# Optimization experiments

Hardware: AMD Instinct MI355X
Metric: run time of the kernel (lower is better)

## Reference

```python
import jax, jax.numpy as jnp
import numpy as np

D_MODEL = 1024
NUM_Q_HEADS = 16
NUM_KV_HEADS = 4
HEAD_DIM = D_MODEL // NUM_Q_HEADS  # 64
B, T = 4, 2048


def _rotate(x):
    # interleaved rotate-half: (x1, x2) pairs -> (-x2, x1)
    x1 = x[..., ::2]
    x2 = x[..., 1::2]
    return jnp.stack((-x2, x1), axis=-1).reshape(x.shape)


def setup_inputs() -> dict:
    key = jax.random.key(0)
    ks = jax.random.split(key, 6)
    x = jax.random.normal(ks[0], (B, T, D_MODEL), dtype=jnp.float32)
    # RoPE tables (precomputed buffers): [T, head_dim]
    pos = jnp.arange(T, dtype=jnp.float32)[:, None]
    inv_freq = 1.0 / (10000.0 ** (jnp.arange(0, HEAD_DIM, 2, dtype=jnp.float32) / HEAD_DIM))
    ang = pos * inv_freq[None, :]                      # [T, head_dim//2]
    ang = jnp.repeat(ang, 2, axis=-1)                  # [T, head_dim]
    cos, sin = jnp.cos(ang), jnp.sin(ang)
    # Linear weights stored as [in, out] (torch y = x @ W.T with W:[out,in]);
    # xavier-uniform scale for a square d_model x d_model layer
    lim = float(np.sqrt(6.0 / (2 * D_MODEL)))
    Wq = jax.random.uniform(ks[1], (D_MODEL, D_MODEL), jnp.float32, -lim, lim)
    kv_out = 2 * NUM_KV_HEADS * HEAD_DIM
    lim_kv = float(np.sqrt(6.0 / (D_MODEL + kv_out)))
    Wkv = jax.random.uniform(ks[2], (D_MODEL, kv_out), jnp.float32, -lim_kv, lim_kv)
    Wo = jax.random.uniform(ks[3], (D_MODEL, D_MODEL), jnp.float32, -lim, lim)
    return {"x": x, "cos": cos, "sin": sin, "Wq": Wq, "Wkv": Wkv, "Wo": Wo}


def reference(x, cos, sin, Wq, Wkv, Wo):
    Bx, Tx, C = x.shape
    hd = HEAD_DIM
    scale = hd ** -0.5
    # projections
    q = (x @ Wq).reshape(Bx, Tx, NUM_Q_HEADS, hd).transpose(0, 2, 1, 3)   # [B,Hq,T,hd]
    kv = (x @ Wkv).reshape(Bx, Tx, NUM_KV_HEADS, 2, hd)
    k = kv[..., 0, :].transpose(0, 2, 1, 3)                               # [B,Hkv,T,hd]
    v = kv[..., 1, :].transpose(0, 2, 1, 3)
    rf = NUM_Q_HEADS // NUM_KV_HEADS
    k = jnp.repeat(k, rf, axis=1)                                         # [B,Hq,T,hd]
    v = jnp.repeat(v, rf, axis=1)
    # inline RoPE on q and k
    c = cos[:Tx, :]
    s = sin[:Tx, :]
    q = q * c + _rotate(q) * s
    k = k * c + _rotate(k) * s
    # full attention (dropout = identity in eval)
    attn = jnp.einsum("bhqd,bhkd->bhqk", q, k) * scale                    # [B,Hq,T,T]
    attn = jax.nn.softmax(attn, axis=-1)
    out = jnp.einsum("bhqk,bhkd->bhqd", attn, v)                          # [B,Hq,T,hd]
    out = out.transpose(0, 2, 1, 3).reshape(Bx, Tx, C)
    return out @ Wo
```

## Files before the change

kernel.cpp:

```cpp
#include <hip/hip_runtime.h>
#include <stdint.h>

constexpr int BATCH = 4;
constexpr int SEQ   = 2048;
constexpr int DM    = 1024;
constexpr int NQH   = 16;
constexpr int NKVH  = 4;
constexpr int HD    = 64;
constexpr int BT    = BATCH * SEQ;

typedef unsigned short u16;
typedef __attribute__((ext_vector_type(4))) unsigned short u16x4;
typedef __attribute__((ext_vector_type(8))) short short8;
typedef __attribute__((ext_vector_type(4))) float f32x4;
typedef __attribute__((ext_vector_type(4))) unsigned int u32x4;

__device__ __forceinline__ unsigned int bf_rne(float f) {
    unsigned int u = __float_as_uint(f);
    u += 0x7fffu + ((u >> 16) & 1u);
    return u >> 16;
}
__device__ __forceinline__ float from_bf(unsigned int h) {
    return __uint_as_float(h << 16);
}
__device__ __forceinline__ void split_bf(float f, u16& hi, u16& lo) {
    unsigned int h = bf_rne(f);
    hi = (u16)h;
    lo = (u16)bf_rne(f - from_bf(h));
}

__device__ __forceinline__ f32x4 mfma16(short8 a, short8 b, f32x4 c) {
    return __builtin_amdgcn_mfma_f32_16x16x32_bf16(a, b, c, 0, 0, 0);
}

typedef const __attribute__((address_space(1))) void gvoid_t;
typedef __attribute__((address_space(3))) void lvoid_t;

__global__ __launch_bounds__(256)
void tsplit_kernel(const float* __restrict__ src, int ldn,
                   u16* __restrict__ dsthi, u16* __restrict__ dstlo)
{
    __shared__ float tl[64][65];
    const int k0 = blockIdx.x * 64, n0 = blockIdx.y * 64;
    const int tid = threadIdx.x;
    #pragma unroll
    for (int p = 0; p < 16; p++) {
        int idx = tid + p * 256;
        int rr = idx >> 6, cc = idx & 63;
        tl[rr][cc] = src[(size_t)(k0 + rr) * ldn + n0 + cc];
    }
    __syncthreads();
    #pragma unroll
    for (int p = 0; p < 16; p++) {
        int idx = tid + p * 256;
        int rr = idx >> 6, cc = idx & 63;
        float v = tl[cc][rr];
        u16 h_, l_;
        split_bf(v, h_, l_);
        dsthi[(size_t)(n0 + rr) * 1024 + k0 + cc] = h_;
        dstlo[(size_t)(n0 + rr) * 1024 + k0 + cc] = l_;
    }
}

template<bool QKV>
__global__ __launch_bounds__(256)
void gemm_mfma(const float* __restrict__ xf,
               const u16* __restrict__ WThi, const u16* __restrict__ WTlo,
               const u16* __restrict__ Bhi,  const u16* __restrict__ Blo,
               const float* __restrict__ cosb, const float* __restrict__ sinb,
               u16* __restrict__ Qhi, u16* __restrict__ Qlo,
               u16* __restrict__ Khi, u16* __restrict__ Klo,
               u16* __restrict__ Vthi, u16* __restrict__ Vtlo,
               float* __restrict__ out)
{
    __shared__ __align__(16) u16 Whs[128 * 64];
    __shared__ __align__(16) u16 Wls[128 * 64];
    __shared__ __align__(16) u16 Xhs[128 * 64];
    __shared__ __align__(16) u16 Xls[128 * 64];

    const int tid  = threadIdx.x;
    const int lane = tid & 63;
    const int w    = tid >> 6;
    const int l15  = lane & 15;
    const int lg   = lane >> 4;
    const int wn   = (w & 1) * 64;
    const int wm   = (w >> 1) * 64;
    const int n0   = blockIdx.x * 128;
    const int m0   = blockIdx.y * 128;

    f32x4 acc[4][4];
    #pragma unroll
    for (int i = 0; i < 4; i++)
        #pragma unroll
        for (int j = 0; j < 4; j++) acc[i][j] = f32x4{0.f, 0.f, 0.f, 0.f};

    for (int k0 = 0; k0 < DM; k0 += 64) {
        __syncthreads();
        if constexpr (QKV) {
            const u16* wsrc = (w < 2) ? WThi : WTlo;
            u16* wdst = (w < 2) ? Whs : Wls;
            #pragma unroll
            for (int it = 0; it < 8; it++) {
                int id = ((w & 1) << 9) | (it << 6) | lane;
                int r = id >> 3, c = id & 7;
                int sc = c ^ (r & 7);
                __builtin_amdgcn_global_load_lds(
                    (gvoid_t*)(wsrc + (size_t)(n0 + r) * 1024 + k0 + sc * 8),
                    (lvoid_t*)(wdst + id * 8), 16, 0, 0);
            }
            int rr = tid >> 1, half = tid & 1;
            const float* xp = xf + (size_t)(m0 + rr) * 1024 + k0 + half * 32;
            float fa[32];
            #pragma unroll
            for (int q = 0; q < 8; q++)
                *reinterpret_cast<float4*>(&fa[q * 4]) =
                    reinterpret_cast<const float4*>(xp)[q];
            #pragma unroll
            for (int c = 0; c < 4; c++) {
                short8 hi8, lo8;
                #pragma unroll
                for (int jj = 0; jj < 8; jj++) {
                    u16 h_, l_;
                    split_bf(fa[c * 8 + jj], h_, l_);
                    hi8[jj] = (short)h_; lo8[jj] = (short)l_;
                }
                int cc = half * 4 + c;
                int sc = cc ^ (rr & 7);
                *reinterpret_cast<short8*>(&Xhs[rr * 64 + sc * 8]) = hi8;
                *reinterpret_cast<short8*>(&Xls[rr * 64 + sc * 8]) = lo8;
            }
        } else {
            const u16* src = (w == 0) ? WThi : (w == 1) ? WTlo : (w == 2) ? Bhi : Blo;
            u16* dst       = (w == 0) ? Whs  : (w == 1) ? Wls  : (w == 2) ? Xhs : Xls;
            int rbase = (w < 2) ? n0 : m0;
            #pragma unroll
            for (int it = 0; it < 16; it++) {
                int id = (it << 6) | lane;
                int r = id >> 3, c = id & 7;
                int sc = c ^ (r & 7);
                __builtin_amdgcn_global_load_lds(
                    (gvoid_t*)(src + (size_t)(rbase + r) * 1024 + k0 + sc * 8),
                    (lvoid_t*)(dst + id * 8), 16, 0, 0);
            }
        }
        __syncthreads();

        #pragma unroll
        for (int ks = 0; ks < 2; ks++) {
            short8 ah[4], al[4], bh[4], bl[4];
            #pragma unroll
            for (int i = 0; i < 4; i++) {
                int rn = wn + i * 16 + l15;
                int ch = ((ks << 2) + lg) ^ (rn & 7);
                ah[i] = *reinterpret_cast<const short8*>(&Whs[rn * 64 + ch * 8]);
                al[i] = *reinterpret_cast<const short8*>(&Wls[rn * 64 + ch * 8]);
            }
            #pragma unroll
            for (int j = 0; j < 4; j++) {
                int rm = wm + j * 16 + l15;
                int ch = ((ks << 2) + lg) ^ (rm & 7);
                bh[j] = *reinterpret_cast<const short8*>(&Xhs[rm * 64 + ch * 8]);
                bl[j] = *reinterpret_cast<const short8*>(&Xls[rm * 64 + ch * 8]);
            }
            #pragma unroll
            for (int i = 0; i < 4; i++)
                #pragma unroll
                for (int j = 0; j < 4; j++) {
                    acc[i][j] = mfma16(ah[i], bh[j], acc[i][j]);
                    acc[i][j] = mfma16(ah[i], bl[j], acc[i][j]);
                    acc[i][j] = mfma16(al[i], bh[j], acc[i][j]);
                }
        }
    }

    if constexpr (QKV) {
        #pragma unroll
        for (int i = 0; i < 4; i++) {
            int nb = n0 + wn + i * 16 + lg * 4;
            if (nb < DM) {
                int hh = nb >> 6, d0 = nb & 63;
                #pragma unroll
                for (int j = 0; j < 4; j++) {
                    int m = m0 + wm + j * 16 + l15;
                    int bb = m >> 11, t = m & (SEQ - 1);
                    float4 c4 = *reinterpret_cast<const float4*>(&cosb[t * HD + d0]);
                    float4 s4 = *reinterpret_cast<const float4*>(&sinb[t * HD + d0]);
                    f32x4 a = acc[i][j];
                    float r0 = (a[0] * c4.x - a[1] * s4.x) * 0.125f;
                    float r1 = (a[1] * c4.x + a[0] * s4.x) * 0.125f;
                    float r2 = (a[2] * c4.z - a[3] * s4.z) * 0.125f;
                    float r3 = (a[3] * c4.z + a[2] * s4.z) * 0.125f;
                    u16 h0, l0, h1, l1, h2, l2, h3, l3;
                    split_bf(r0, h0, l0); split_bf(r1, h1, l1);
                    split_bf(r2, h2, l2); split_bf(r3, h3, l3);
                    size_t off = ((size_t)(bb * NQH + hh) * SEQ + t) * HD + d0;
                    *reinterpret_cast<u16x4*>(&Qhi[off]) = u16x4{h0, h1, h2, h3};
                    *reinterpret_cast<u16x4*>(&Qlo[off]) = u16x4{l0, l1, l2, l3};
                }
            } else {
                int rem = nb - DM;
                int kvh = rem >> 7, r2v = rem & 127;
                if (r2v < HD) {
                    int d0 = r2v;
                    #pragma unroll
                    for (int j = 0; j < 4; j++) {
                        int m = m0 + wm + j * 16 + l15;
                        int bb = m >> 11, t = m & (SEQ - 1);
                        float4 c4 = *reinterpret_cast<const float4*>(&cosb[t * HD + d0]);
                        float4 s4 = *reinterpret_cast<const float4*>(&sinb[t * HD + d0]);
                        f32x4 a = acc[i][j];
                        float r0 = a[0] * c4.x - a[1] * s4.x;
                        float r1 = a[1] * c4.x + a[0] * s4.x;
                        float r2 = a[2] * c4.z - a[3] * s4.z;
                        float r3 = a[3] * c4.z + a[2] * s4.z;
                        u16 h0, l0, h1, l1, h2, l2, h3, l3;
                        split_bf(r0, h0, l0); split_bf(r1, h1, l1);
                        split_bf(r2, h2, l2); split_bf(r3, h3, l3);
                        size_t off = ((size_t)(bb * NKVH + kvh) * SEQ + t) * HD + d0;
                        *reinterpret_cast<u16x4*>(&Khi[off]) = u16x4{h0, h1, h2, h3};
                        *reinterpret_cast<u16x4*>(&Klo[off]) = u16x4{l0, l1, l2, l3};
                    }
                } else {
                    int d0 = r2v - HD;
                    #pragma unroll
                    for (int j = 0; j < 4; j++) {
                        int m = m0 + wm + j * 16 + l15;
                        int bb = m >> 11, t = m & (SEQ - 1);
                        size_t vb = (size_t)(bb * NKVH + kvh) * HD;
                        #pragma unroll
                        for (int reg = 0; reg < 4; reg++) {
                            u16 hv, lv;
                            split_bf(acc[i][j][reg], hv, lv);
                            size_t off = (vb + d0 + reg) * SEQ + t;
                            Vthi[off] = hv; Vtlo[off] = lv;
                        }
                    }
                }
            }
        }
    } else {
        #pragma unroll
        for (int i = 0; i < 4; i++) {
            int nb = n0 + wn + i * 16 + lg * 4;
            #pragma unroll
            for (int j = 0; j < 4; j++) {
                int m = m0 + wm + j * 16 + l15;
                *reinterpret_cast<float4*>(&out[(size_t)m * DM + nb]) =
                    make_float4(acc[i][j][0], acc[i][j][1], acc[i][j][2], acc[i][j][3]);
            }
        }
    }
}

__global__ __launch_bounds__(256)
void attn_kernel(const u16* __restrict__ Qhi, const u16* __restrict__ Qlo,
                 const u16* __restrict__ Khi, const u16* __restrict__ Klo,
                 const u16* __restrict__ Vthi, const u16* __restrict__ Vtlo,
                 u16* __restrict__ AOhi, u16* __restrict__ AOlo)
{
    __shared__ __align__(16) u16 Kh[64 * 64];
    __shared__ __align__(16) u16 Kl[64 * 64];
    __shared__ __align__(16) u16 Vh[64 * 64];
    __shared__ __align__(16) u16 Vl[64 * 64];
    __shared__ __align__(16) unsigned int Pb[4][16 * 64];

    const int tid  = threadIdx.x;
    const int lane = tid & 63;
    const int w    = tid >> 6;
    const int l15  = lane & 15;
    const int lg   = lane >> 4;

    const int qt  = blockIdx.x;
    const int bh  = blockIdx.y;
    const int bb  = bh >> 4, h = bh & 15;
    const int kvh = h >> 2;

    const size_t qoff = ((size_t)(bb * NQH + h) * SEQ + qt * 64 + w * 16 + l15) * HD + lg * 8;
    short8 qh[2], ql[2];
    qh[0] = *reinterpret_cast<const short8*>(Qhi + qoff);
    qh[1] = *reinterpret_cast<const short8*>(Qhi + qoff + 32);
    ql[0] = *reinterpret_cast<const short8*>(Qlo + qoff);
    ql[1] = *reinterpret_cast<const short8*>(Qlo + qoff + 32);

    const u16* gb = (w == 0) ? Khi : (w == 1) ? Klo : (w == 2) ? Vthi : Vtlo;
    u16* lb       = (w == 0) ? Kh  : (w == 1) ? Kl  : (w == 2) ? Vh   : Vl;
    const bool isK = (w < 2);
    const size_t ktstep = isK ? (size_t)(64 * HD) : (size_t)64;
    size_t loff[8];
    {
        size_t kb = (size_t)(bb * NKVH + kvh) * SEQ;
        size_t vb = (size_t)(bb * NKVH + kvh) * HD;
        #pragma unroll
        for (int it = 0; it < 8; it++) {
            int nn = it * 64 + lane;
            int r  = nn >> 3, c = nn & 7;
            int sc = c ^ (r & 7);
            loff[it] = isK ? ((kb + r) * (size_t)HD + sc * 8)
                           : ((vb + r) * (size_t)SEQ + sc * 8);
        }
    }

    f32x4 oA[4] = {{0,0,0,0},{0,0,0,0},{0,0,0,0},{0,0,0,0}};
    float mrow[4] = {-1e30f,-1e30f,-1e30f,-1e30f};
    float lrow[4] = {0.f,0.f,0.f,0.f};

    for (int kt = 0; kt < SEQ / 64; kt++) {
        __syncthreads();
        #pragma unroll
        for (int it = 0; it < 8; it++) {
            __builtin_amdgcn_global_load_lds(
                (gvoid_t*)(gb + loff[it] + (size_t)kt * ktstep),
                (lvoid_t*)(lb + it * 512), 16, 0, 0);
        }
        __syncthreads();

        f32x4 sA[4];
        #pragma unroll
        for (int ct = 0; ct < 4; ct++) {
            f32x4 s = {0.f, 0.f, 0.f, 0.f};
            #pragma unroll
            for (int ks = 0; ks < 2; ks++) {
                int r = ct * 16 + l15;
                int c = (ks * 4 + lg) ^ (r & 7);
                short8 kh = *reinterpret_cast<const short8*>(Kh + r * 64 + c * 8);
                short8 kl = *reinterpret_cast<const short8*>(Kl + r * 64 + c * 8);
                s = mfma16(qh[ks], kh, s);
                s = mfma16(qh[ks], kl, s);
                s = mfma16(ql[ks], kh, s);
            }
            sA[ct] = s;
        }

        #pragma unroll
        for (int rr = 0; rr < 4; rr++) {
            float mx = fmaxf(fmaxf(sA[0][rr], sA[1][rr]), fmaxf(sA[2][rr], sA[3][rr]));
            mx = fmaxf(mx, __shfl_xor(mx, 1));
            mx = fmaxf(mx, __shfl_xor(mx, 2));
            mx = fmaxf(mx, __shfl_xor(mx, 4));
            mx = fmaxf(mx, __shfl_xor(mx, 8));
            float mnew = fmaxf(mrow[rr], mx);
            float corr = __expf(mrow[rr] - mnew);
            mrow[rr] = mnew;
            const int prow = lg * 4 + rr;
            float ps = 0.f;
            #pragma unroll
            for (int ct = 0; ct < 4; ct++) {
                float p = __expf(sA[ct][rr] - mnew);
                ps += p;
                unsigned int hb = bf_rne(p);
                unsigned int lbits = bf_rne(p - from_bf(hb));
                int colS = (ct * 16 + l15) ^ ((prow & 7) << 3);
                Pb[w][prow * 64 + colS] = hb | (lbits << 16);
            }
            ps += __shfl_xor(ps, 1);
            ps += __shfl_xor(ps, 2);
            ps += __shfl_xor(ps, 4);
            ps += __shfl_xor(ps, 8);
            lrow[rr] = lrow[rr] * corr + ps;
            oA[0][rr] *= corr; oA[1][rr] *= corr; oA[2][rr] *= corr; oA[3][rr] *= corr;
        }

        short8 pah[2], pal[2];
        #pragma unroll
        for (int ks = 0; ks < 2; ks++) {
            int colS = (ks * 32 + lg * 8) ^ ((l15 & 7) << 3);
            const u32x4* pp = reinterpret_cast<const u32x4*>(&Pb[w][l15 * 64 + colS]);
            u32x4 u0 = pp[0], u1 = pp[1];
            #pragma unroll
            for (int j = 0; j < 4; j++) {
                pah[ks][j]     = (short)(u0[j] & 0xffffu);
                pal[ks][j]     = (short)(u0[j] >> 16);
                pah[ks][4 + j] = (short)(u1[j] & 0xffffu);
                pal[ks][4 + j] = (short)(u1[j] >> 16);
            }
        }
        #pragma unroll
        for (int dt = 0; dt < 4; dt++) {
            f32x4 o = oA[dt];
            #pragma unroll
            for (int ks = 0; ks < 2; ks++) {
                int d = dt * 16 + l15;
                int c = (ks * 4 + lg) ^ (d & 7);
                short8 vh = *reinterpret_cast<const short8*>(Vh + d * 64 + c * 8);
                short8 vl = *reinterpret_cast<const short8*>(Vl + d * 64 + c * 8);
                o = mfma16(pah[ks], vh, o);
                o = mfma16(pah[ks], vl, o);
                o = mfma16(pal[ks], vh, o);
            }
            oA[dt] = o;
        }
    }

    #pragma unroll
    for (int rr = 0; rr < 4; rr++) {
        float inv = 1.f / lrow[rr];
        int qrow = qt * 64 + w * 16 + lg * 4 + rr;
        size_t off = ((size_t)bb * SEQ + qrow) * DM + h * 64 + l15;
        #pragma unroll
        for (int dt = 0; dt < 4; dt++) {
            float v = oA[dt][rr] * inv;
            unsigned int hb = bf_rne(v);
            AOhi[off + dt * 16] = (u16)hb;
            AOlo[off + dt * 16] = (u16)bf_rne(v - from_bf(hb));
        }
    }
}

extern "C" void kernel_launch(void* const* d_in, const int* in_sizes, int n_in,
                              void* d_out, int out_size, void* d_ws, size_t ws_size,
                              hipStream_t stream)
{
    const float* x    = (const float*)d_in[0];
    const float* cosb = (const float*)d_in[1];
    const float* sinb = (const float*)d_in[2];
    const float* Wq   = (const float*)d_in[3];
    const float* Wkv  = (const float*)d_in[4];
    const float* Wo   = (const float*)d_in[5];
    float* out = (float*)d_out;

    u16* base  = (u16*)d_ws;
    u16* AOhi  = base;
    u16* AOlo  = base + 8388608;
    u16* WThi  = base;
    u16* WTlo  = base + 1572864;
    u16* Qhi   = base + 16777216;
    u16* Qlo   = base + 25165824;
    u16* WoThi = base + 16777216;
    u16* WoTlo = base + 17825792;
    u16* Khi   = base + 33554432;
    u16* Klo   = base + 35651584;
    u16* Vthi  = base + 37748736;
    u16* Vtlo  = base + 39845888;

    tsplit_kernel<<<dim3(16, 16), 256, 0, stream>>>(Wq, 1024, WThi, WTlo);
    tsplit_kernel<<<dim3(16, 8),  256, 0, stream>>>(Wkv, 512, WThi + 1048576, WTlo + 1048576);

    gemm_mfma<true><<<dim3(12, 64), 256, 0, stream>>>(
        x, WThi, WTlo, nullptr, nullptr, cosb, sinb,
        Qhi, Qlo, Khi, Klo, Vthi, Vtlo, nullptr);

    attn_kernel<<<dim3(32, 64), 256, 0, stream>>>(
        Qhi, Qlo, Khi, Klo, Vthi, Vtlo, AOhi, AOlo);

    tsplit_kernel<<<dim3(16, 16), 256, 0, stream>>>(Wo, 1024, WoThi, WoTlo);

    gemm_mfma<false><<<dim3(8, 64), 256, 0, stream>>>(
        nullptr, WoThi, WoTlo, AOhi, AOlo, nullptr, nullptr,
        nullptr, nullptr, nullptr, nullptr, nullptr, nullptr, out);
}
```

Measured before the change: 641.1 us.

## Transpose QK^T MFMA to make softmax per-lane and add lo*lo precision term

The S=QK^T MFMA operands are swapped so each lane holds one query row's scores. That lets the online softmax max and sum use only two cross-lane shuffles instead of per-row 4-step reductions. P is written to LDS as one 128-bit store per tile instead of scalar stores, and the per-row correction and normalizer are fetched with shuffles. A fourth lo*lo MFMA term is also added to the projection GEMM, the QK and the PV products, which raises MFMA work by about a third in exchange for extra accuracy.

```diff
diff --git a/kernel.cpp b/kernel.cpp
--- a/kernel.cpp
+++ b/kernel.cpp
@@ -169,6 +169,7 @@
                     acc[i][j] = mfma16(ah[i], bh[j], acc[i][j]);
                     acc[i][j] = mfma16(ah[i], bl[j], acc[i][j]);
                     acc[i][j] = mfma16(al[i], bh[j], acc[i][j]);
+                    acc[i][j] = mfma16(al[i], bl[j], acc[i][j]);
                 }
         }
     }
@@ -301,8 +302,8 @@
     }
 
     f32x4 oA[4] = {{0,0,0,0},{0,0,0,0},{0,0,0,0},{0,0,0,0}};
-    float mrow[4] = {-1e30f,-1e30f,-1e30f,-1e30f};
-    float lrow[4] = {0.f,0.f,0.f,0.f};
+    float mstate = -1e30f;
+    float lstate = 0.f;
 
     for (int kt = 0; kt < SEQ / 64; kt++) {
         __syncthreads();
@@ -324,40 +325,52 @@
                 int c = (ks * 4 + lg) ^ (r & 7);
                 short8 kh = *reinterpret_cast<const short8*>(Kh + r * 64 + c * 8);
                 short8 kl = *reinterpret_cast<const short8*>(Kl + r * 64 + c * 8);
-                s = mfma16(qh[ks], kh, s);
-                s = mfma16(qh[ks], kl, s);
-                s = mfma16(ql[ks], kh, s);
+                s = mfma16(kh, qh[ks], s);
+                s = mfma16(kh, ql[ks], s);
+                s = mfma16(kl, qh[ks], s);
+                s = mfma16(kl, ql[ks], s);
             }
             sA[ct] = s;
         }
 
-        #pragma unroll
-        for (int rr = 0; rr < 4; rr++) {
-            float mx = fmaxf(fmaxf(sA[0][rr], sA[1][rr]), fmaxf(sA[2][rr], sA[3][rr]));
-            mx = fmaxf(mx, __shfl_xor(mx, 1));
-            mx = fmaxf(mx, __shfl_xor(mx, 2));
-            mx = fmaxf(mx, __shfl_xor(mx, 4));
-            mx = fmaxf(mx, __shfl_xor(mx, 8));
-            float mnew = fmaxf(mrow[rr], mx);
-            float corr = __expf(mrow[rr] - mnew);
-            mrow[rr] = mnew;
-            const int prow = lg * 4 + rr;
-            float ps = 0.f;
-            #pragma unroll
-            for (int ct = 0; ct < 4; ct++) {
-                float p = __expf(sA[ct][rr] - mnew);
+        float tmx = sA[0][0];
+        #pragma unroll
+        for (int ct = 0; ct < 4; ct++)
+            #pragma unroll
+            for (int r = 0; r < 4; r++) tmx = fmaxf(tmx, sA[ct][r]);
+        tmx = fmaxf(tmx, __shfl_xor(tmx, 16));
+        tmx = fmaxf(tmx, __shfl_xor(tmx, 32));
+        float mnew = fmaxf(mstate, tmx);
+        float corr = __expf(mstate - mnew);
+        mstate = mnew;
+
+        float ps = 0.f;
+        u32x4 pk[4];
+        #pragma unroll
+        for (int ct = 0; ct < 4; ct++) {
+            #pragma unroll
+            for (int r = 0; r < 4; r++) {
+                float p = __expf(sA[ct][r] - mnew);
                 ps += p;
                 unsigned int hb = bf_rne(p);
-                unsigned int lbits = bf_rne(p - from_bf(hb));
-                int colS = (ct * 16 + l15) ^ ((prow & 7) << 3);
-                Pb[w][prow * 64 + colS] = hb | (lbits << 16);
-            }
-            ps += __shfl_xor(ps, 1);
-            ps += __shfl_xor(ps, 2);
-            ps += __shfl_xor(ps, 4);
-            ps += __shfl_xor(ps, 8);
-            lrow[rr] = lrow[rr] * corr + ps;
-            oA[0][rr] *= corr; oA[1][rr] *= corr; oA[2][rr] *= corr; oA[3][rr] *= corr;
+                pk[ct][r] = hb | (bf_rne(p - from_bf(hb)) << 16);
+            }
+        }
+        ps += __shfl_xor(ps, 16);
+        ps += __shfl_xor(ps, 32);
+        lstate = lstate * corr + ps;
+
+        #pragma unroll
+        for (int ct = 0; ct < 4; ct++) {
+            int c8 = ct * 2 + (lg >> 1);
+            int colS = ((c8 ^ (l15 & 7)) << 3) | ((lg & 1) << 2);
+            *reinterpret_cast<u32x4*>(&Pb[w][l15 * 64 + colS]) = pk[ct];
+        }
+
+        #pragma unroll
+        for (int rr = 0; rr < 4; rr++) {
+            float c4 = __shfl(corr, lg * 4 + rr, 16);
+            oA[0][rr] *= c4; oA[1][rr] *= c4; oA[2][rr] *= c4; oA[3][rr] *= c4;
         }
 
         short8 pah[2], pal[2];
@@ -386,6 +399,7 @@
                 o = mfma16(pah[ks], vh, o);
                 o = mfma16(pah[ks], vl, o);
                 o = mfma16(pal[ks], vh, o);
+                o = mfma16(pal[ks], vl, o);
             }
             oA[dt] = o;
         }
@@ -393,7 +407,8 @@
 
     #pragma unroll
     for (int rr = 0; rr < 4; rr++) {
-        float inv = 1.f / lrow[rr];
+        float lfin = __shfl(lstate, lg * 4 + rr, 16);
+        float inv = 1.f / lfin;
         int qrow = qt * 64 + w * 16 + lg * 4 + rr;
         size_t off = ((size_t)bb * SEQ + qrow) * DM + h * 64 + l15;
         #pragma unroll
```

After: 594.5 us. 1.08x faster.
